# Optimization experiments

Hardware: AMD Instinct MI355X
Metric: run time of the kernel (lower is better)

The kernel has to match this reference:

```python
import jax, jax.numpy as jnp
import numpy as np

B, T, D = 4, 2048, 1024
RANK, FACTOR, SUB = 8, 64, 4
S = 4 * SUB  # 16


def construct_hamilton(A):
    # A: [rank, 4, sub, sub] -> [rank, 4*sub, 4*sub]
    r, i, j, k = A[:, 0], A[:, 1], A[:, 2], A[:, 3]
    return jnp.concatenate([
        jnp.concatenate([r, -i, -j, -k], axis=2),
        jnp.concatenate([i, r, -k, j], axis=2),
        jnp.concatenate([j, k, r, -i], axis=2),
        jnp.concatenate([k, -j, i, r], axis=2),
    ], axis=1)


def setup_inputs() -> dict:
    key = jax.random.key(0)
    k1, k2, k3 = jax.random.split(key, 3)
    x = jax.random.normal(k1, (B, T, D), dtype=jnp.float32)
    A = jax.random.normal(k2, (RANK, 4, SUB, SUB), dtype=jnp.float32)
    # orthogonal-ish init with (r+1)^-0.5 scaling, like the torch init
    fB = jax.random.normal(k3, (RANK, FACTOR, FACTOR), dtype=jnp.float32)
    q, _ = jnp.linalg.qr(fB)
    scale = (jnp.arange(RANK, dtype=jnp.float32) + 1.0) ** -0.5
    factors_B = q * scale[:, None, None]
    bias = jnp.zeros((D,), dtype=jnp.float32)
    return {"x": x, "A": A, "factors_B": factors_B, "bias": bias}


def reference(x, A, factors_B, bias):
    Bb, Tt, Dd = x.shape
    x_flat = x.reshape(-1, S, FACTOR)          # [N, s, i]
    H = construct_hamilton(A)                   # [r, k, s]
    wav = jnp.einsum('nsi,rji->rnsj', x_flat, factors_B)  # [r, N, s, j]
    out = jnp.einsum('rnsj,rks->nkj', wav, H)   # [N, k, j]
    return out.reshape(Bb, Tt, Dd) + bias
```

## Files before the change

### kernel.cpp

```cpp
#include <hip/hip_runtime.h>
#include <stdint.h>

#define RANKS 8
#define MDIM 8192
#define KDIM 1024
#define NDIM 1024
#define BM 256
#define BN 128
#define BK 64
#define NT (KDIM / BK)
#define THREADS 512

typedef __bf16 bf16x8 __attribute__((ext_vector_type(8)));
typedef unsigned short u16x8 __attribute__((ext_vector_type(8)));
typedef float f32x4 __attribute__((ext_vector_type(4)));

__device__ __forceinline__ unsigned short f2bf(float f) {
  union { float f; uint32_t u; } v; v.f = f;
  uint32_t u = v.u;
  u += 0x7FFFu + ((u >> 16) & 1u);
  return (unsigned short)(u >> 16);
}

__constant__ int   c_comp[4][4] = {{0,1,2,3},{1,0,3,2},{2,3,0,1},{3,2,1,0}};
__constant__ float c_sign[4][4] = {{1.f,-1.f,-1.f,-1.f},
                                   {1.f, 1.f,-1.f, 1.f},
                                   {1.f, 1.f, 1.f,-1.f},
                                   {1.f,-1.f, 1.f, 1.f}};

__global__ void build_W(const float* __restrict__ A, const float* __restrict__ fB,
                        unsigned short* __restrict__ W) {
  int idx = blockIdx.x * 256 + threadIdx.x;
  int p  = idx >> 8;
  int q4 = (idx & 255) << 2;
  int k = p >> 6, j = p & 63;
  int kb = k >> 2, ks = k & 3;
  int s = q4 >> 6;
  int sb = s >> 2, ss = s & 3;
  int   comp = c_comp[kb][sb];
  float sgn  = c_sign[kb][sb];
  float o0 = 0.f, o1 = 0.f, o2 = 0.f, o3 = 0.f;
  int i0 = q4 & 63;
#pragma unroll
  for (int r = 0; r < RANKS; ++r) {
    float h = sgn * A[r * 64 + comp * 16 + ks * 4 + ss];
    const float* fb = fB + r * 4096 + j * 64 + i0;
    o0 += h * fb[0]; o1 += h * fb[1]; o2 += h * fb[2]; o3 += h * fb[3];
  }
  ushort4 st;
  st.x = f2bf(o0); st.y = f2bf(o1); st.z = f2bf(o2); st.w = f2bf(o3);
  *reinterpret_cast<ushort4*>(W + (size_t)p * KDIM + q4) = st;
}

__device__ __forceinline__ void gload16(const unsigned short* g, unsigned short* l) {
  __builtin_amdgcn_global_load_lds(
      (const __attribute__((address_space(1))) unsigned int*)(uintptr_t)g,
      (__attribute__((address_space(3))) unsigned int*)(uintptr_t)l,
      16, 0, 0);
}

#define SWZ(r, cbyte) (((r) * 128) + ((cbyte) ^ (((r) & 7) << 4)))

__global__ __launch_bounds__(THREADS, 2) void gemm_ham(
    const float* __restrict__ x, const unsigned short* __restrict__ W,
    const float* __restrict__ bias, float* __restrict__ out) {
  __shared__ unsigned short Asm_[2][BM * BK];
  __shared__ unsigned short Bsm_[3][BN * BK];

  const int tid  = threadIdx.x;
  const int lane = tid & 63;
  const int wid  = tid >> 6;
  const int wr   = wid >> 1;
  const int wc   = wid & 1;
  const int rb   = lane & 15;
  const int qtr  = lane >> 4;

  const int flat = blockIdx.x;
  const int xg = flat & 7, ig = flat >> 3;
  const int bx = xg * 4 + (ig >> 3);
  const int by = ig & 7;
  const int row0 = bx * BM;
  const int col0 = by * BN;

  f32x4 acc[4][4];
  f32x4 zero = {0.f, 0.f, 0.f, 0.f};
#pragma unroll
  for (int m = 0; m < 4; ++m)
#pragma unroll
    for (int n = 0; n < 4; ++n) acc[m][n] = zero;

  float4 arE[8], arO[8];

  auto loadA = [&](int kt, float4 (&ar)[8]) {
    const int k0 = kt * BK;
#pragma unroll
    for (int g = 0; g < 4; ++g) {
      int id = g * 512 + tid;
      int r = id >> 3, c8 = (id & 7) << 3;
      const float* src = x + (size_t)(row0 + r) * KDIM + k0 + c8;
      ar[2 * g]     = *reinterpret_cast<const float4*>(src);
      ar[2 * g + 1] = *reinterpret_cast<const float4*>(src + 4);
    }
  };
  auto writeA = [&](unsigned short* dst, const float4 (&ar)[8]) {
#pragma unroll
    for (int g = 0; g < 4; ++g) {
      int id = g * 512 + tid;
      int r = id >> 3, c8 = (id & 7) << 3;
      bf16x8 v;
      v[0] = (__bf16)ar[2*g].x;   v[1] = (__bf16)ar[2*g].y;
      v[2] = (__bf16)ar[2*g].z;   v[3] = (__bf16)ar[2*g].w;
      v[4] = (__bf16)ar[2*g+1].x; v[5] = (__bf16)ar[2*g+1].y;
      v[6] = (__bf16)ar[2*g+1].z; v[7] = (__bf16)ar[2*g+1].w;
      *reinterpret_cast<bf16x8*>(
          reinterpret_cast<char*>(dst) + SWZ(r, c8 * 2)) = v;
    }
  };
  auto stageB = [&](int kt, int slot) {
    unsigned short* dst = &Bsm_[slot][0];
#pragma unroll
    for (int g = 0; g < 2; ++g) {
      int id = g * 512 + tid;
      int r = id >> 3, ct = id & 7;
      gload16(W + (size_t)(col0 + r) * KDIM + kt * BK + ((ct ^ (r & 7)) << 3),
              dst + id * 8);
    }
  };

  auto tile = [&](int t, const unsigned short* Ard, unsigned short* Awr,
                  float4 (&arLd)[8], float4 (&arWr)[8], int scur, int sstage) {
    const bool doStage = (t + 2 < NT);
    const bool doWrite = (t + 1 < NT);
    if (doStage) {
      loadA(t + 2, arLd);
      stageB(t + 2, sstage);
    }
    __builtin_amdgcn_sched_barrier(0);
    const unsigned short* Brd = &Bsm_[0][0] + scur * (BN * BK);
    __builtin_amdgcn_s_setprio(1);
#pragma unroll
    for (int kk = 0; kk < 2; ++kk) {
      const int cb = (qtr * 8 + kk * 32) * 2;
      bf16x8 af[4], bfr[4];
#pragma unroll
      for (int m = 0; m < 4; ++m) {
        int r = wr * 64 + m * 16 + rb;
        af[m] = *reinterpret_cast<const bf16x8*>(
            reinterpret_cast<const char*>(Ard) + SWZ(r, cb));
      }
#pragma unroll
      for (int n = 0; n < 4; ++n) {
        int r = wc * 64 + n * 16 + rb;
        bfr[n] = *reinterpret_cast<const bf16x8*>(
            reinterpret_cast<const char*>(Brd) + SWZ(r, cb));
      }
#pragma unroll
      for (int m = 0; m < 4; ++m)
#pragma unroll
        for (int n = 0; n < 4; ++n)
          acc[m][n] = __builtin_amdgcn_mfma_f32_16x16x32_bf16(af[m], bfr[n], acc[m][n], 0, 0, 0);
    }
    __builtin_amdgcn_s_setprio(0);
    if (doWrite) writeA(Awr, arWr);
    __builtin_amdgcn_sched_barrier(0);
    if (t < NT - 1) {
      if (doStage) asm volatile("s_waitcnt vmcnt(10)" ::: "memory");
      else         asm volatile("s_waitcnt vmcnt(0)"  ::: "memory");
      asm volatile("s_waitcnt lgkmcnt(0)" ::: "memory");
      __builtin_amdgcn_sched_barrier(0);
      __builtin_amdgcn_s_barrier();
      __builtin_amdgcn_sched_barrier(0);
    }
  };

  loadA(0, arE);
  writeA(&Asm_[0][0], arE);
  stageB(0, 0);
  loadA(1, arO);
  stageB(1, 1);
  asm volatile("s_waitcnt vmcnt(10)" ::: "memory");
  asm volatile("s_waitcnt lgkmcnt(0)" ::: "memory");
  __builtin_amdgcn_sched_barrier(0);
  __builtin_amdgcn_s_barrier();
  __builtin_amdgcn_sched_barrier(0);

  int sc = 0;
#pragma unroll 1
  for (int t2 = 0; t2 < NT; t2 += 2) {
    int ss0 = (sc == 0) ? 2 : sc - 1;
    tile(t2, &Asm_[0][0], &Asm_[1][0], arE, arO, sc, ss0);
    sc = (sc == 2) ? 0 : sc + 1;
    int ss1 = (sc == 0) ? 2 : sc - 1;
    tile(t2 + 1, &Asm_[1][0], &Asm_[0][0], arO, arE, sc, ss1);
    sc = (sc == 2) ? 0 : sc + 1;
  }

  const int crow = row0 + wr * 64 + qtr * 4;
  const int ccol = col0 + wc * 64 + rb;
#pragma unroll
  for (int n = 0; n < 4; ++n) {
    int c = ccol + n * 16;
    float bv = bias[c];
#pragma unroll
    for (int m = 0; m < 4; ++m)
#pragma unroll
      for (int v = 0; v < 4; ++v)
        out[(size_t)(crow + m * 16 + v) * NDIM + c] = acc[m][n][v] + bv;
  }
}

__global__ void fallback_kernel(const float* __restrict__ x, const float* __restrict__ A,
                                const float* __restrict__ fB, const float* __restrict__ bias,
                                float* __restrict__ out) {
  __shared__ float xrow[1024];
  const int n = blockIdx.x;
  const int tid = threadIdx.x;
  for (int t = tid; t < 1024; t += 256) xrow[t] = x[(size_t)n * 1024 + t];
  __syncthreads();
  for (int pp = 0; pp < 4; ++pp) {
    int p = pp * 256 + tid;
    int k = p >> 6, j = p & 63;
    int kb = k >> 2, ks = k & 3;
    float accv = 0.f;
    for (int s = 0; s < 16; ++s) {
      int sb = s >> 2, ss = s & 3;
      int comp = c_comp[kb][sb];
      float sgn = c_sign[kb][sb];
      float hA[RANKS];
#pragma unroll
      for (int r = 0; r < RANKS; ++r) hA[r] = sgn * A[r * 64 + comp * 16 + ks * 4 + ss];
      for (int i = 0; i < 64; ++i) {
        float w = 0.f;
#pragma unroll
        for (int r = 0; r < RANKS; ++r) w += hA[r] * fB[r * 4096 + j * 64 + i];
        accv += xrow[s * 64 + i] * w;
      }
    }
    out[(size_t)n * 1024 + p] = accv + bias[p];
  }
}

extern "C" void kernel_launch(void* const* d_in, const int* in_sizes, int n_in,
                              void* d_out, int out_size, void* d_ws, size_t ws_size,
                              hipStream_t stream) {
  const float* x    = (const float*)d_in[0];
  const float* A    = (const float*)d_in[1];
  const float* fB   = (const float*)d_in[2];
  const float* bias = (const float*)d_in[3];
  float* out = (float*)d_out;

  const size_t needW = (size_t)NDIM * KDIM * sizeof(unsigned short);
  if (ws_size >= needW) {
    unsigned short* W = (unsigned short*)d_ws;
    build_W<<<dim3(1024), dim3(256), 0, stream>>>(A, fB, W);
    gemm_ham<<<dim3((MDIM / BM) * (NDIM / BN)), dim3(THREADS), 0, stream>>>(x, W, bias, out);
  } else {
    fallback_kernel<<<dim3(MDIM), dim3(256), 0, stream>>>(x, A, fB, bias, out);
  }
}
```

Measured before the change: 36.51 us.

## Split each K-tile into two phases interleaving global loads and LDS writes

The GEMM main loop is restructured so each 64-wide K tile runs as two half-K MFMA phases. The A-tile global loads, B-tile async LDS staging and bf16 conversion writes are split into halves, one half issued inside each phase, with barriers between phases. The prologue now preloads and writes both A buffers up front. The aim is to spread memory traffic more evenly across the MFMA work instead of bunching it at tile boundaries, at the cost of extra workgroup barriers per tile.

```diff
diff --git a/kernel.cpp b/kernel.cpp
--- a/kernel.cpp
+++ b/kernel.cpp
@@ -91,108 +91,129 @@
 
   float4 arE[8], arO[8];
 
-  auto loadA = [&](int kt, float4 (&ar)[8]) {
-    const int k0 = kt * BK;
-#pragma unroll
-    for (int g = 0; g < 4; ++g) {
-      int id = g * 512 + tid;
-      int r = id >> 3, c8 = (id & 7) << 3;
-      const float* src = x + (size_t)(row0 + r) * KDIM + k0 + c8;
-      ar[2 * g]     = *reinterpret_cast<const float4*>(src);
-      ar[2 * g + 1] = *reinterpret_cast<const float4*>(src + 4);
-    }
-  };
-  auto writeA = [&](unsigned short* dst, const float4 (&ar)[8]) {
-#pragma unroll
-    for (int g = 0; g < 4; ++g) {
-      int id = g * 512 + tid;
-      int r = id >> 3, c8 = (id & 7) << 3;
-      bf16x8 v;
-      v[0] = (__bf16)ar[2*g].x;   v[1] = (__bf16)ar[2*g].y;
-      v[2] = (__bf16)ar[2*g].z;   v[3] = (__bf16)ar[2*g].w;
-      v[4] = (__bf16)ar[2*g+1].x; v[5] = (__bf16)ar[2*g+1].y;
-      v[6] = (__bf16)ar[2*g+1].z; v[7] = (__bf16)ar[2*g+1].w;
-      *reinterpret_cast<bf16x8*>(
-          reinterpret_cast<char*>(dst) + SWZ(r, c8 * 2)) = v;
-    }
-  };
-  auto stageB = [&](int kt, int slot) {
-    unsigned short* dst = &Bsm_[slot][0];
-#pragma unroll
-    for (int g = 0; g < 2; ++g) {
-      int id = g * 512 + tid;
-      int r = id >> 3, ct = id & 7;
-      gload16(W + (size_t)(col0 + r) * KDIM + kt * BK + ((ct ^ (r & 7)) << 3),
-              dst + id * 8);
-    }
-  };
-
-  auto tile = [&](int t, const unsigned short* Ard, unsigned short* Awr,
-                  float4 (&arLd)[8], float4 (&arWr)[8], int scur, int sstage) {
-    const bool doStage = (t + 2 < NT);
-    const bool doWrite = (t + 1 < NT);
-    if (doStage) {
-      loadA(t + 2, arLd);
-      stageB(t + 2, sstage);
-    }
+  auto loadAg = [&](int kt, int g, float4& r0, float4& r1) {
+    int id = g * 512 + tid;
+    int r = id >> 3, c8 = (id & 7) << 3;
+    const float* src = x + (size_t)(row0 + r) * KDIM + kt * BK + c8;
+    r0 = *reinterpret_cast<const float4*>(src);
+    r1 = *reinterpret_cast<const float4*>(src + 4);
+  };
+  auto writeAg = [&](unsigned short* dst, int g, const float4& r0, const float4& r1) {
+    int id = g * 512 + tid;
+    int r = id >> 3, c8 = (id & 7) << 3;
+    bf16x8 v;
+    v[0] = (__bf16)r0.x; v[1] = (__bf16)r0.y; v[2] = (__bf16)r0.z; v[3] = (__bf16)r0.w;
+    v[4] = (__bf16)r1.x; v[5] = (__bf16)r1.y; v[6] = (__bf16)r1.z; v[7] = (__bf16)r1.w;
+    *reinterpret_cast<bf16x8*>(reinterpret_cast<char*>(dst) + SWZ(r, c8 * 2)) = v;
+  };
+  auto stageBg = [&](int kt, unsigned short* dst, int g) {
+    int id = g * 512 + tid;
+    int r = id >> 3, ct = id & 7;
+    gload16(W + (size_t)(col0 + r) * KDIM + kt * BK + ((ct ^ (r & 7)) << 3),
+            dst + id * 8);
+  };
+
+  auto do_phase = [&](const unsigned short* Ard, const unsigned short* Brd, int kk,
+                      auto&& stg) {
+    bf16x8 af[4], bfr[4];
+    const int cb = qtr * 16 + kk * 64;
+#pragma unroll
+    for (int m = 0; m < 4; ++m)
+      af[m] = *reinterpret_cast<const bf16x8*>(
+          reinterpret_cast<const char*>(Ard) + SWZ(wr * 64 + m * 16 + rb, cb));
+#pragma unroll
+    for (int n = 0; n < 4; ++n)
+      bfr[n] = *reinterpret_cast<const bf16x8*>(
+          reinterpret_cast<const char*>(Brd) + SWZ(wc * 64 + n * 16 + rb, cb));
+    stg();
     __builtin_amdgcn_sched_barrier(0);
-    const unsigned short* Brd = &Bsm_[0][0] + scur * (BN * BK);
+    __builtin_amdgcn_s_barrier();
+    asm volatile("s_waitcnt lgkmcnt(0)" ::: "memory");
+    __builtin_amdgcn_sched_barrier(0);
     __builtin_amdgcn_s_setprio(1);
 #pragma unroll
-    for (int kk = 0; kk < 2; ++kk) {
-      const int cb = (qtr * 8 + kk * 32) * 2;
-      bf16x8 af[4], bfr[4];
-#pragma unroll
-      for (int m = 0; m < 4; ++m) {
-        int r = wr * 64 + m * 16 + rb;
-        af[m] = *reinterpret_cast<const bf16x8*>(
-            reinterpret_cast<const char*>(Ard) + SWZ(r, cb));
-      }
-#pragma unroll
-      for (int n = 0; n < 4; ++n) {
-        int r = wc * 64 + n * 16 + rb;
-        bfr[n] = *reinterpret_cast<const bf16x8*>(
-            reinterpret_cast<const char*>(Brd) + SWZ(r, cb));
-      }
-#pragma unroll
-      for (int m = 0; m < 4; ++m)
-#pragma unroll
-        for (int n = 0; n < 4; ++n)
-          acc[m][n] = __builtin_amdgcn_mfma_f32_16x16x32_bf16(af[m], bfr[n], acc[m][n], 0, 0, 0);
-    }
+    for (int m = 0; m < 4; ++m)
+#pragma unroll
+      for (int n = 0; n < 4; ++n)
+        acc[m][n] = __builtin_amdgcn_mfma_f32_16x16x32_bf16(af[m], bfr[n], acc[m][n], 0, 0, 0);
     __builtin_amdgcn_s_setprio(0);
-    if (doWrite) writeA(Awr, arWr);
     __builtin_amdgcn_sched_barrier(0);
-    if (t < NT - 1) {
-      if (doStage) asm volatile("s_waitcnt vmcnt(10)" ::: "memory");
-      else         asm volatile("s_waitcnt vmcnt(0)"  ::: "memory");
-      asm volatile("s_waitcnt lgkmcnt(0)" ::: "memory");
-      __builtin_amdgcn_sched_barrier(0);
-      __builtin_amdgcn_s_barrier();
-      __builtin_amdgcn_sched_barrier(0);
-    }
-  };
-
-  loadA(0, arE);
-  writeA(&Asm_[0][0], arE);
-  stageB(0, 0);
-  loadA(1, arO);
-  stageB(1, 1);
-  asm volatile("s_waitcnt vmcnt(10)" ::: "memory");
+  };
+
+  loadAg(0, 0, arE[0], arE[1]); loadAg(0, 1, arE[2], arE[3]);
+  loadAg(0, 2, arE[4], arE[5]); loadAg(0, 3, arE[6], arE[7]);
+  loadAg(1, 0, arO[0], arO[1]); loadAg(1, 1, arO[2], arO[3]);
+  loadAg(1, 2, arO[4], arO[5]); loadAg(1, 3, arO[6], arO[7]);
+  stageBg(0, &Bsm_[0][0], 0); stageBg(0, &Bsm_[0][0], 1);
+  stageBg(1, &Bsm_[1][0], 0); stageBg(1, &Bsm_[1][0], 1);
+  writeAg(&Asm_[0][0], 0, arE[0], arE[1]); writeAg(&Asm_[0][0], 1, arE[2], arE[3]);
+  writeAg(&Asm_[0][0], 2, arE[4], arE[5]); writeAg(&Asm_[0][0], 3, arE[6], arE[7]);
+  writeAg(&Asm_[1][0], 0, arO[0], arO[1]); writeAg(&Asm_[1][0], 1, arO[2], arO[3]);
+  writeAg(&Asm_[1][0], 2, arO[4], arO[5]); writeAg(&Asm_[1][0], 3, arO[6], arO[7]);
+  asm volatile("s_waitcnt vmcnt(0)" ::: "memory");
   asm volatile("s_waitcnt lgkmcnt(0)" ::: "memory");
   __builtin_amdgcn_sched_barrier(0);
   __builtin_amdgcn_s_barrier();
   __builtin_amdgcn_sched_barrier(0);
 
-  int sc = 0;
+  int scur = 0;
 #pragma unroll 1
-  for (int t2 = 0; t2 < NT; t2 += 2) {
-    int ss0 = (sc == 0) ? 2 : sc - 1;
-    tile(t2, &Asm_[0][0], &Asm_[1][0], arE, arO, sc, ss0);
-    sc = (sc == 2) ? 0 : sc + 1;
-    int ss1 = (sc == 0) ? 2 : sc - 1;
-    tile(t2 + 1, &Asm_[1][0], &Asm_[0][0], arO, arE, sc, ss1);
-    sc = (sc == 2) ? 0 : sc + 1;
+  for (int t = 0; t < NT; t += 2) {
+    {
+      const unsigned short* Ard = &Asm_[0][0];
+      unsigned short*       Awr = &Asm_[1][0];
+      const unsigned short* Brd = &Bsm_[0][0] + scur * (BN * BK);
+      int sst = scur + 2; if (sst >= 3) sst -= 3;
+      unsigned short*       Bst = &Bsm_[0][0] + sst * (BN * BK);
+      const bool dl = (t + 2 < NT);
+      const bool dw = (t >= 1);
+      do_phase(Ard, Brd, 0, [&] {
+        if (dl) { loadAg(t + 2, 0, arE[0], arE[1]); loadAg(t + 2, 1, arE[2], arE[3]);
+                  stageBg(t + 2, Bst, 0); }
+        if (dw) { writeAg(Awr, 0, arO[0], arO[1]); writeAg(Awr, 1, arO[2], arO[3]); }
+      });
+      __builtin_amdgcn_s_barrier();
+      do_phase(Ard, Brd, 1, [&] {
+        if (dl) { loadAg(t + 2, 2, arE[4], arE[5]); loadAg(t + 2, 3, arE[6], arE[7]);
+                  stageBg(t + 2, Bst, 1); }
+        if (dw) { writeAg(Awr, 2, arO[4], arO[5]); writeAg(Awr, 3, arO[6], arO[7]); }
+      });
+      if (dl) asm volatile("s_waitcnt vmcnt(10)" ::: "memory");
+      else    asm volatile("s_waitcnt vmcnt(0)"  ::: "memory");
+      __builtin_amdgcn_sched_barrier(0);
+      __builtin_amdgcn_s_barrier();
+      __builtin_amdgcn_sched_barrier(0);
+      scur = scur + 1; if (scur >= 3) scur -= 3;
+    }
+    {
+      const int to = t + 1;
+      const unsigned short* Ard = &Asm_[1][0];
+      unsigned short*       Awr = &Asm_[0][0];
+      const unsigned short* Brd = &Bsm_[0][0] + scur * (BN * BK);
+      int sst = scur + 2; if (sst >= 3) sst -= 3;
+      unsigned short*       Bst = &Bsm_[0][0] + sst * (BN * BK);
+      const bool dl = (to + 2 < NT);
+      const bool dw = (to + 1 < NT);
+      do_phase(Ard, Brd, 0, [&] {
+        if (dl) { loadAg(to + 2, 0, arO[0], arO[1]); loadAg(to + 2, 1, arO[2], arO[3]);
+                  stageBg(to + 2, Bst, 0); }
+        if (dw) { writeAg(Awr, 0, arE[0], arE[1]); writeAg(Awr, 1, arE[2], arE[3]); }
+      });
+      __builtin_amdgcn_s_barrier();
+      do_phase(Ard, Brd, 1, [&] {
+        if (dl) { loadAg(to + 2, 2, arO[4], arO[5]); loadAg(to + 2, 3, arO[6], arO[7]);
+                  stageBg(to + 2, Bst, 1); }
+        if (dw) { writeAg(Awr, 2, arE[4], arE[5]); writeAg(Awr, 3, arE[6], arE[7]); }
+      });
+      if (to + 1 < NT) {
+        if (dl) asm volatile("s_waitcnt vmcnt(10)" ::: "memory");
+        else    asm volatile("s_waitcnt vmcnt(0)"  ::: "memory");
+        __builtin_amdgcn_sched_barrier(0);
+        __builtin_amdgcn_s_barrier();
+        __builtin_amdgcn_sched_barrier(0);
+      }
+      scur = scur + 1; if (scur >= 3) scur -= 3;
+    }
   }
 
   const int crow = row0 + wr * 64 + qtr * 4;
```

Result: slower. 47.34 us (+29.7%).
